# Kernel tuning notes

Measured on AMD Instinct MI355X. Metric: run time of the kernel, lower is better.

Reference implementation:

```python
import math
import jax, jax.numpy as jnp
import numpy as np

B, T, C = 2, 384, 768
NH, RANK = 384, 1          # code requires rank==1 and num_heads==T (block_size)
HD = C // NH               # head dim = 2
SCALE = (1.0 / math.sqrt(HD)) * (RANK ** 0.5)
LN_EPS = 1e-5


def _layernorm(x, g, b):
    m = jnp.mean(x, axis=-1, keepdims=True)
    v = jnp.mean(jnp.square(x - m), axis=-1, keepdims=True)
    return (x - m) * jax.lax.rsqrt(v + LN_EPS) * g + b


def setup_inputs() -> dict:
    key = jax.random.key(0)
    ks = jax.random.split(key, 8)
    s = 0.02
    return {
        "x": jax.random.normal(ks[0], (B, T, C), jnp.float32),
        "W_qkv": jax.random.normal(ks[1], (C, 3 * C), jnp.float32) * s,
        "b_qkv": jnp.zeros((3 * C,), jnp.float32),
        "W_proj": jax.random.normal(ks[2], (C, C), jnp.float32) * s,
        "b_proj": jnp.zeros((C,), jnp.float32),
        "ln1_g": jnp.ones((C,), jnp.float32),
        "ln1_b": jnp.zeros((C,), jnp.float32),
        "ln2_g": jnp.ones((C,), jnp.float32),
        "ln2_b": jnp.zeros((C,), jnp.float32),
        "W1": jax.random.normal(ks[3], (C, 4 * C), jnp.float32) * s,
        "b1": jnp.zeros((4 * C,), jnp.float32),
        "W2": jax.random.normal(ks[4], (4 * C, C), jnp.float32) * s,
        "b2": jnp.zeros((C,), jnp.float32),
    }


def reference(x, W_qkv, b_qkv, W_proj, b_proj, ln1_g, ln1_b, ln2_g, ln2_b, W1, b1, W2, b2):
    # --- attention branch (pre-LN) ---
    h = _layernorm(x, ln1_g, ln1_b)
    qkv = h @ W_qkv + b_qkv                       # [B,T,3C]
    q, k, v = jnp.split(qkv, 3, axis=-1)

    def split_heads(t):                           # [B,T,C] -> [B,RANK,T,NH,HD]
        return t.reshape(B, T, RANK, NH, HD).transpose(0, 2, 1, 3, 4)

    q, k, v = split_heads(q), split_heads(k), split_heads(v)
    # scores over the HEAD axis (nh x nh), per (batch, rank, time) -- faithful to source
    att = jnp.einsum('brtnd,brtmd->brtnm', q, k) * SCALE   # [B,RANK,T,NH,NH]
    tril = jnp.tril(jnp.ones((T, T), bool))       # NH == T so this broadcasts on (nh, nh)
    att = jnp.where(tril, att, -jnp.inf)
    att = jax.nn.softmax(att, axis=-1)
    y = jnp.einsum('brtnm,brtmd->brtnd', att, v)  # [B,RANK,T,NH,HD]
    y = y.transpose(0, 2, 1, 3, 4).reshape(B, T, C)
    x = x + (y @ W_proj + b_proj)

    # --- feed-forward branch: Linear -> Linear -> GELU (order faithful to source) ---
    h2 = _layernorm(x, ln2_g, ln2_b)
    ff = jax.nn.gelu((h2 @ W1 + b1) @ W2 + b2, approximate=False)
    return x + ff
```

## Files before the change

kernel.cpp:

```cpp
#include <hip/hip_runtime.h>
#include <hip/hip_bf16.h>
#include <math.h>

#define SCALE_QK 0.70710678118654752f
#define PSTRIDE 589824

typedef __attribute__((ext_vector_type(8))) short bf16x8;
typedef __attribute__((ext_vector_type(4))) float floatx4;

__device__ __forceinline__ void gload16(const void* g, void* l) {
  __builtin_amdgcn_global_load_lds(
      (const __attribute__((address_space(1))) void*)g,
      (__attribute__((address_space(3))) void*)l, 16, 0, 0);
}

__device__ __forceinline__ float bf2f(unsigned short u) {
  union { float f; unsigned int i; } c; c.i = ((unsigned int)u) << 16; return c.f;
}

__device__ __forceinline__ float gelu_f(float v) {
  return 0.5f * v * (1.f + erff(v * 0.70710678118654752f));
}

struct MegaArgs {
  const float *x, *Wq, *bq, *Wp, *bp, *g1, *be1, *g2, *be2, *W1, *b1, *W2, *b2;
  __hip_bfloat16 *h1, *qkvb, *yb, *h2, *ff1b, *Tq, *Tp, *T1, *T2;
  float *x2, *part, *out;
};

__device__ __forceinline__ void wconv_seg(const float* __restrict__ src,
                                          __hip_bfloat16* __restrict__ dst,
                                          int K, int N, int idx, char* smem) {
  float (*t)[33] = (float(*)[33])smem;
  int tilesN = N >> 5;
  int tk = idx / tilesN, tn = idx - tk * tilesN;
  int r = threadIdx.x >> 5, c = threadIdx.x & 31;
#pragma unroll
  for (int p = 0; p < 4; ++p)
    t[p * 8 + r][c] = src[(size_t)(tk * 32 + p * 8 + r) * N + tn * 32 + c];
  __syncthreads();
#pragma unroll
  for (int p = 0; p < 4; ++p)
    dst[(size_t)(tn * 32 + p * 8 + r) * K + tk * 32 + c] =
        __float2bfloat16(t[c][p * 8 + r]);
}

__device__ __forceinline__ void ln_row(const float* __restrict__ src,
                                       const float* __restrict__ g,
                                       const float* __restrict__ b,
                                       __hip_bfloat16* __restrict__ dst,
                                       int r, char* smem) {
  float* red0 = (float*)smem; float* red1 = red0 + 4;
  const float* xr = src + (size_t)r * 768;
  __hip_bfloat16* orow = dst + (size_t)r * 768;
  float vals[3]; float s = 0.f, s2 = 0.f;
#pragma unroll
  for (int p = 0; p < 3; ++p) {
    float v = xr[threadIdx.x + p * 256];
    vals[p] = v; s += v; s2 += v * v;
  }
#pragma unroll
  for (int off = 32; off > 0; off >>= 1) {
    s += __shfl_down(s, off); s2 += __shfl_down(s2, off);
  }
  int wid = threadIdx.x >> 6, lane = threadIdx.x & 63;
  if (lane == 0) { red0[wid] = s; red1[wid] = s2; }
  __syncthreads();
  if (threadIdx.x == 0) {
    red0[0] = red0[0] + red0[1] + red0[2] + red0[3];
    red1[0] = red1[0] + red1[1] + red1[2] + red1[3];
  }
  __syncthreads();
  float mean = red0[0] * (1.f / 768), var = red1[0] * (1.f / 768) - mean * mean;
  float rstd = rsqrtf(var + 1e-5f);
#pragma unroll
  for (int p = 0; p < 3; ++p) {
    int i = threadIdx.x + p * 256;
    orow[i] = __float2bfloat16((vals[p] - mean) * rstd * g[i] + b[i]);
  }
}

template <int NT, bool GELU, bool RES, bool OUT_BF16, bool SPLIT>
__device__ __forceinline__ void gemm_tile(
    const __hip_bfloat16* __restrict__ A, int ldA,
    const __hip_bfloat16* __restrict__ Bt, int ldB,
    const float* __restrict__ bias, const float* __restrict__ res,
    void* __restrict__ outp, int N, int bm, int bn, int kofe, char* lds) {
  const int tid = threadIdx.x;
  const int w = tid >> 6, l = tid & 63;

  const int sr = (w << 3) + (l >> 3);
  const int swb = ((l & 7) << 4) ^ ((l >> 3) << 4);
  const char* a0 = (const char*)(A + (size_t)(bm + sr) * ldA + kofe) + swb;
  const char* a1 = a0 + (size_t)32 * ldA * 2;
  const char* b0 = (const char*)(Bt + (size_t)(bn + sr) * ldB + kofe) + swb;
  const char* b1 = b0 + (size_t)32 * ldB * 2;
  char* dW = lds + (w << 10);

#define STAGE(buf, t) do {                     \
    char* d_ = dW + (buf) * 16384;             \
    gload16(a0 + (t) * 128, d_);               \
    gload16(a1 + (t) * 128, d_ + 4096);        \
    gload16(b0 + (t) * 128, d_ + 8192);        \
    gload16(b1 + (t) * 128, d_ + 12288);       \
  } while (0)

  const int wr = w >> 1, wc = w & 1;
  const int fr = l & 15, g = l >> 4;
  const int fsw = (fr & 7) << 4;
  int aof[2][2], bof[2][2];
#pragma unroll
  for (int i = 0; i < 2; ++i)
#pragma unroll
    for (int kk = 0; kk < 2; ++kk) {
      aof[i][kk] = (wr * 32 + i * 16 + fr) * 128 + ((kk * 64 + g * 16) ^ fsw);
      bof[i][kk] = 8192 + (wc * 32 + i * 16 + fr) * 128 +
                   ((kk * 64 + g * 16) ^ fsw);
    }

  floatx4 acc[2][2] = {};

#define COMPUTE(bufoff) do {                                          \
    const char* base_ = lds + (bufoff);                               \
    bf16x8 av_[2][2], bv_[2][2];                                      \
    _Pragma("unroll") for (int i = 0; i < 2; ++i)                     \
      _Pragma("unroll") for (int kk = 0; kk < 2; ++kk) {              \
        av_[i][kk] = *(const bf16x8*)(base_ + aof[i][kk]);            \
        bv_[i][kk] = *(const bf16x8*)(base_ + bof[i][kk]);            \
      }                                                               \
    _Pragma("unroll") for (int kk = 0; kk < 2; ++kk)                  \
      _Pragma("unroll") for (int i = 0; i < 2; ++i)                   \
        _Pragma("unroll") for (int j = 0; j < 2; ++j)                 \
          acc[i][j] = __builtin_amdgcn_mfma_f32_16x16x32_bf16(        \
              av_[i][kk], bv_[j][kk], acc[i][j], 0, 0, 0);            \
  } while (0)

  STAGE(0, 0);
  STAGE(1, 1);
  asm volatile("s_waitcnt vmcnt(4)" ::: "memory");
  __builtin_amdgcn_s_barrier();
  asm volatile("" ::: "memory");

#pragma unroll
  for (int t = 0; t < NT; ++t) {
    if (t + 2 < NT) STAGE((t + 2) % 3, t + 2);
    COMPUTE((t % 3) * 16384);
    if (t + 1 < NT) {
      if (t + 2 < NT) {
        asm volatile("s_waitcnt vmcnt(4)" ::: "memory");
      } else {
        asm volatile("s_waitcnt vmcnt(0)" ::: "memory");
      }
      __builtin_amdgcn_s_barrier();
      asm volatile("" ::: "memory");
    }
  }
#undef STAGE
#undef COMPUTE

  const int orow0 = bm + wr * 32 + g * 4;
  const int ocol0 = bn + wc * 32 + fr;
#pragma unroll
  for (int fm = 0; fm < 2; ++fm)
#pragma unroll
    for (int fn = 0; fn < 2; ++fn) {
      int col = ocol0 + fn * 16;
      float bv = SPLIT ? 0.f : bias[col];
#pragma unroll
      for (int i = 0; i < 4; ++i) {
        int row = orow0 + fm * 16 + i;
        if (SPLIT) {
          ((float*)outp)[(size_t)row * N + col] = acc[fm][fn][i];
        } else {
          float v = acc[fm][fn][i] + bv;
          if (GELU) v = gelu_f(v);
          if (RES) v += res[(size_t)row * N + col];
          if (OUT_BF16)
            ((__hip_bfloat16*)outp)[(size_t)row * N + col] = __float2bfloat16(v);
          else
            ((float*)outp)[(size_t)row * N + col] = v;
        }
      }
    }
}

__device__ __forceinline__ void attn_row(int n, const ushort2* base,
    const float2* ks, const float2* vs, __hip_bfloat16* yrow) {
  ushort2 qu = base[n];
  float q0 = bf2f(qu.x) * SCALE_QK, q1 = bf2f(qu.y) * SCALE_QK;
  float sm = 0.f, y0 = 0.f, y1 = 0.f;
  for (int m = 0; m <= n; ++m) {
    float2 km = ks[m], vm = vs[m];
    float p = __expf(fmaf(q0, km.x, q1 * km.y));
    sm += p;
    y0 = fmaf(p, vm.x, y0);
    y1 = fmaf(p, vm.y, y1);
  }
  float inv = 1.f / sm;
  yrow[2 * n]     = __float2bfloat16(y0 * inv);
  yrow[2 * n + 1] = __float2bfloat16(y1 * inv);
}

__device__ __forceinline__ void attn_token(int r, const MegaArgs& a, char* smem) {
  float2* ks = (float2*)smem;
  float2* vs = ks + 384;
  const int t = threadIdx.x;
  const ushort2* base = (const ushort2*)(a.qkvb + (size_t)r * 2304);
  {
    ushort2 ku = base[384 + t], vu = base[768 + t];
    ks[t] = make_float2(bf2f(ku.x), bf2f(ku.y));
    vs[t] = make_float2(bf2f(vu.x), bf2f(vu.y));
    if (t < 128) {
      ushort2 ku2 = base[384 + 256 + t], vu2 = base[768 + 256 + t];
      ks[256 + t] = make_float2(bf2f(ku2.x), bf2f(ku2.y));
      vs[256 + t] = make_float2(bf2f(vu2.x), bf2f(vu2.y));
    }
  }
  __syncthreads();
  __hip_bfloat16* yrow = a.yb + (size_t)r * 768;
  attn_row(t, base, ks, vs, yrow);
  if (t < 128) attn_row(383 - t, base, ks, vs, yrow);
}

__device__ __forceinline__ void p7_elem(int idx, const MegaArgs& a) {
  int i = idx * 4;
  floatx4 s = *(const floatx4*)(a.part + i);
  s += *(const floatx4*)(a.part + PSTRIDE + i);
  s += *(const floatx4*)(a.part + 2 * (size_t)PSTRIDE + i);
  s += *(const floatx4*)(a.part + 3 * (size_t)PSTRIDE + i);
  int c = i - (i / 768) * 768;
  floatx4 bv = *(const floatx4*)(a.b2 + c);
  floatx4 xv = *(const floatx4*)(a.x2 + i);
  floatx4 o;
#pragma unroll
  for (int e = 0; e < 4; ++e) o[e] = xv[e] + gelu_f(s[e] + bv[e]);
  *(floatx4*)(a.out + i) = o;
}

__global__ __launch_bounds__(256) void p0_k(MegaArgs a) {
  __shared__ __align__(16) char smem[8448];
  int j = blockIdx.x;
  if (j < 1728) wconv_seg(a.Wq, a.Tq, 768, 2304, j, smem);
  else          ln_row(a.x, a.g1, a.be1, a.h1, j - 1728, smem);
}
__global__ __launch_bounds__(256) void p1_k(MegaArgs a) {
  __shared__ __align__(16) char smem[49152];
  int j = blockIdx.x;
  if (j < 432) {
    int bm = (j / 36) << 6, bn = (j % 36) << 6;
    gemm_tile<12, false, false, true, false>(
        a.h1, 768, a.Tq, 768, a.bq, nullptr, a.qkvb, 2304, bm, bn, 0, smem);
  } else {
    int jj = j - 432;
    if (jj < 576)       wconv_seg(a.Wp, a.Tp, 768, 768, jj, smem);
    else if (jj < 2880) wconv_seg(a.W1, a.T1, 768, 3072, jj - 576, smem);
    else                wconv_seg(a.W2, a.T2, 3072, 768, jj - 2880, smem);
  }
}
__global__ __launch_bounds__(256) void p2_k(MegaArgs a) {
  __shared__ __align__(16) char smem[6144];
  attn_token(blockIdx.x, a, smem);
}
__global__ __launch_bounds__(256) void p3_k(MegaArgs a) {
  __shared__ __align__(16) char smem[49152];
  int j = blockIdx.x;
  int bm = (j / 12) << 6, bn = (j % 12) << 6;
  gemm_tile<12, false, true, false, false>(
      a.yb, 768, a.Tp, 768, a.bp, a.x, a.x2, 768, bm, bn, 0, smem);
}
__global__ __launch_bounds__(256) void p4_k(MegaArgs a) {
  __shared__ __align__(16) char smem[64];
  ln_row(a.x2, a.g2, a.be2, a.h2, blockIdx.x, smem);
}
__global__ __launch_bounds__(256) void p5_k(MegaArgs a) {
  __shared__ __align__(16) char smem[49152];
  int j = blockIdx.x;
  int bm = (j / 48) << 6, bn = (j % 48) << 6;
  gemm_tile<12, false, false, true, false>(
      a.h2, 768, a.T1, 768, a.b1, nullptr, a.ff1b, 3072, bm, bn, 0, smem);
}
__global__ __launch_bounds__(256) void p6_k(MegaArgs a) {
  __shared__ __align__(16) char smem[49152];
  int j = blockIdx.x;
  int z = j / 144, r2 = j - z * 144;
  int bm = (r2 / 12) << 6, bn = (r2 % 12) << 6;
  gemm_tile<12, false, false, false, true>(
      a.ff1b, 3072, a.T2, 3072, nullptr, nullptr,
      a.part + (size_t)z * PSTRIDE, 768, bm, bn, z * 768, smem);
}
__global__ __launch_bounds__(256) void p7_k(MegaArgs a) {
  p7_elem(blockIdx.x * 256 + threadIdx.x, a);
}

extern "C" void kernel_launch(void* const* d_in, const int* in_sizes, int n_in,
                              void* d_out, int out_size, void* d_ws,
                              size_t ws_size, hipStream_t stream) {
  (void)in_sizes; (void)n_in; (void)out_size; (void)ws_size;
  MegaArgs a;
  a.x   = (const float*)d_in[0];
  a.Wq  = (const float*)d_in[1];
  a.bq  = (const float*)d_in[2];
  a.Wp  = (const float*)d_in[3];
  a.bp  = (const float*)d_in[4];
  a.g1  = (const float*)d_in[5];
  a.be1 = (const float*)d_in[6];
  a.g2  = (const float*)d_in[7];
  a.be2 = (const float*)d_in[8];
  a.W1  = (const float*)d_in[9];
  a.b1  = (const float*)d_in[10];
  a.W2  = (const float*)d_in[11];
  a.b2  = (const float*)d_in[12];

  char* p = (char*)d_ws;
  a.h1   = (__hip_bfloat16*)p; p += 768 * 768 * 2;
  a.qkvb = (__hip_bfloat16*)p; p += 768 * 2304 * 2;
  a.yb   = (__hip_bfloat16*)p; p += 768 * 768 * 2;
  a.x2   = (float*)p;          p += 768 * 768 * 4;
  a.h2   = (__hip_bfloat16*)p; p += 768 * 768 * 2;
  a.ff1b = (__hip_bfloat16*)p; p += 768 * 3072 * 2;
  a.Tq   = (__hip_bfloat16*)p; p += 2304 * 768 * 2;
  a.Tp   = (__hip_bfloat16*)p; p += 768 * 768 * 2;
  a.T1   = (__hip_bfloat16*)p; p += 3072 * 768 * 2;
  a.T2   = (__hip_bfloat16*)p; p += 768 * 3072 * 2;
  a.part = (float*)p;          p += 4 * 768 * 768 * 4;
  a.out  = (float*)d_out;

  p0_k<<<2496, 256, 0, stream>>>(a);
  p1_k<<<5616, 256, 0, stream>>>(a);
  p2_k<<<768, 256, 0, stream>>>(a);
  p3_k<<<144, 256, 0, stream>>>(a);
  p4_k<<<768, 256, 0, stream>>>(a);
  p5_k<<<576, 256, 0, stream>>>(a);
  p6_k<<<576, 256, 0, stream>>>(a);
  p7_k<<<576, 256, 0, stream>>>(a);
}
```

Before: 85.90 us.

## Fuse LN2 and final GELU epilogue into GEMMs via last-block atomic counters

Removes the standalone LN2 and split-K reduction/GELU kernels. Each proj-GEMM row panel counts finished tiles with an atomic counter, and the last tile block runs layernorm for that 64-row panel. Likewise, the last of the four split-K partial blocks for each output tile reduces the partials and applies bias, GELU and the residual. This cuts two kernel launches and their gaps, at the cost of serialized tail work in the winning blocks and a counter reset added to the first kernel.

```diff
diff --git a/kernel.cpp b/kernel.cpp
--- a/kernel.cpp
+++ b/kernel.cpp
@@ -26,6 +26,7 @@
   const float *x, *Wq, *bq, *Wp, *bp, *g1, *be1, *g2, *be2, *W1, *b1, *W2, *b2;
   __hip_bfloat16 *h1, *qkvb, *yb, *h2, *ff1b, *Tq, *Tp, *T1, *T2;
   float *x2, *part, *out;
+  int *cnt;
 };
 
 __device__ __forceinline__ void wconv_seg(const float* __restrict__ src,
@@ -77,6 +78,53 @@
   for (int p = 0; p < 3; ++p) {
     int i = threadIdx.x + p * 256;
     orow[i] = __float2bfloat16((vals[p] - mean) * rstd * g[i] + b[i]);
+  }
+}
+
+__device__ __forceinline__ void ln_panel(const MegaArgs& a, int bm) {
+  const int sub = threadIdx.x & 3;
+  const int row = bm + (threadIdx.x >> 2);
+  const float* xr = a.x2 + (size_t)row * 768 + sub * 192;
+  float s = 0.f, s2 = 0.f;
+#pragma unroll
+  for (int i = 0; i < 48; ++i) {
+    floatx4 v = *(const floatx4*)(xr + i * 4);
+#pragma unroll
+    for (int e = 0; e < 4; ++e) { s += v[e]; s2 += v[e] * v[e]; }
+  }
+  s += __shfl_xor(s, 1); s2 += __shfl_xor(s2, 1);
+  s += __shfl_xor(s, 2); s2 += __shfl_xor(s2, 2);
+  float mean = s * (1.f / 768), var = s2 * (1.f / 768) - mean * mean;
+  float rstd = rsqrtf(var + 1e-5f);
+  __hip_bfloat16* orow = a.h2 + (size_t)row * 768 + sub * 192;
+  const float* g = a.g2 + sub * 192;
+  const float* b = a.be2 + sub * 192;
+#pragma unroll
+  for (int i = 0; i < 48; ++i) {
+    floatx4 v = *(const floatx4*)(xr + i * 4);
+#pragma unroll
+    for (int e = 0; e < 4; ++e)
+      orow[i * 4 + e] =
+          __float2bfloat16((v[e] - mean) * rstd * g[i * 4 + e] + b[i * 4 + e]);
+  }
+}
+
+__device__ __forceinline__ void ff2_finish(const MegaArgs& a, int bm, int bn) {
+#pragma unroll
+  for (int q = 0; q < 4; ++q) {
+    int e4 = q * 256 + threadIdx.x;
+    int r = e4 >> 4, c4 = e4 & 15;
+    size_t off = (size_t)(bm + r) * 768 + bn + c4 * 4;
+    floatx4 s = *(const floatx4*)(a.part + off);
+    s += *(const floatx4*)(a.part + PSTRIDE + off);
+    s += *(const floatx4*)(a.part + 2 * (size_t)PSTRIDE + off);
+    s += *(const floatx4*)(a.part + 3 * (size_t)PSTRIDE + off);
+    floatx4 bv = *(const floatx4*)(a.b2 + bn + c4 * 4);
+    floatx4 xv = *(const floatx4*)(a.x2 + off);
+    floatx4 o;
+#pragma unroll
+    for (int e = 0; e < 4; ++e) o[e] = xv[e] + gelu_f(s[e] + bv[e]);
+    *(floatx4*)(a.out + off) = o;
   }
 }
 
@@ -222,26 +270,12 @@
   if (t < 128) attn_row(383 - t, base, ks, vs, yrow);
 }
 
-__device__ __forceinline__ void p7_elem(int idx, const MegaArgs& a) {
-  int i = idx * 4;
-  floatx4 s = *(const floatx4*)(a.part + i);
-  s += *(const floatx4*)(a.part + PSTRIDE + i);
-  s += *(const floatx4*)(a.part + 2 * (size_t)PSTRIDE + i);
-  s += *(const floatx4*)(a.part + 3 * (size_t)PSTRIDE + i);
-  int c = i - (i / 768) * 768;
-  floatx4 bv = *(const floatx4*)(a.b2 + c);
-  floatx4 xv = *(const floatx4*)(a.x2 + i);
-  floatx4 o;
-#pragma unroll
-  for (int e = 0; e < 4; ++e) o[e] = xv[e] + gelu_f(s[e] + bv[e]);
-  *(floatx4*)(a.out + i) = o;
-}
-
 __global__ __launch_bounds__(256) void p0_k(MegaArgs a) {
   __shared__ __align__(16) char smem[8448];
   int j = blockIdx.x;
-  if (j < 1728) wconv_seg(a.Wq, a.Tq, 768, 2304, j, smem);
-  else          ln_row(a.x, a.g1, a.be1, a.h1, j - 1728, smem);
+  if (j < 1728)      wconv_seg(a.Wq, a.Tq, 768, 2304, j, smem);
+  else if (j < 2496) ln_row(a.x, a.g1, a.be1, a.h1, j - 1728, smem);
+  else if (threadIdx.x < 156) a.cnt[threadIdx.x] = 0;
 }
 __global__ __launch_bounds__(256) void p1_k(MegaArgs a) {
   __shared__ __align__(16) char smem[49152];
@@ -263,33 +297,44 @@
 }
 __global__ __launch_bounds__(256) void p3_k(MegaArgs a) {
   __shared__ __align__(16) char smem[49152];
+  __shared__ int winner;
   int j = blockIdx.x;
   int bm = (j / 12) << 6, bn = (j % 12) << 6;
   gemm_tile<12, false, true, false, false>(
       a.yb, 768, a.Tp, 768, a.bp, a.x, a.x2, 768, bm, bn, 0, smem);
+  __syncthreads();
+  __threadfence();
+  if (threadIdx.x == 0) winner = atomicAdd(&a.cnt[bm >> 6], 1);
+  __syncthreads();
+  if (winner == 11) {
+    __threadfence();
+    ln_panel(a, bm);
+  }
 }
 __global__ __launch_bounds__(256) void p4_k(MegaArgs a) {
-  __shared__ __align__(16) char smem[64];
-  ln_row(a.x2, a.g2, a.be2, a.h2, blockIdx.x, smem);
-}
-__global__ __launch_bounds__(256) void p5_k(MegaArgs a) {
   __shared__ __align__(16) char smem[49152];
   int j = blockIdx.x;
   int bm = (j / 48) << 6, bn = (j % 48) << 6;
   gemm_tile<12, false, false, true, false>(
       a.h2, 768, a.T1, 768, a.b1, nullptr, a.ff1b, 3072, bm, bn, 0, smem);
 }
-__global__ __launch_bounds__(256) void p6_k(MegaArgs a) {
+__global__ __launch_bounds__(256) void p5_k(MegaArgs a) {
   __shared__ __align__(16) char smem[49152];
+  __shared__ int winner;
   int j = blockIdx.x;
   int z = j / 144, r2 = j - z * 144;
   int bm = (r2 / 12) << 6, bn = (r2 % 12) << 6;
   gemm_tile<12, false, false, false, true>(
       a.ff1b, 3072, a.T2, 3072, nullptr, nullptr,
       a.part + (size_t)z * PSTRIDE, 768, bm, bn, z * 768, smem);
-}
-__global__ __launch_bounds__(256) void p7_k(MegaArgs a) {
-  p7_elem(blockIdx.x * 256 + threadIdx.x, a);
+  __syncthreads();
+  __threadfence();
+  if (threadIdx.x == 0) winner = atomicAdd(&a.cnt[12 + r2], 1);
+  __syncthreads();
+  if (winner == 3) {
+    __threadfence();
+    ff2_finish(a, bm, bn);
+  }
 }
 
 extern "C" void kernel_launch(void* const* d_in, const int* in_sizes, int n_in,
@@ -323,14 +368,13 @@
   a.T1   = (__hip_bfloat16*)p; p += 3072 * 768 * 2;
   a.T2   = (__hip_bfloat16*)p; p += 768 * 3072 * 2;
   a.part = (float*)p;          p += 4 * 768 * 768 * 4;
+  a.cnt  = (int*)p;            p += 156 * 4;
   a.out  = (float*)d_out;
 
-  p0_k<<<2496, 256, 0, stream>>>(a);
+  p0_k<<<2497, 256, 0, stream>>>(a);
   p1_k<<<5616, 256, 0, stream>>>(a);
   p2_k<<<768, 256, 0, stream>>>(a);
   p3_k<<<144, 256, 0, stream>>>(a);
-  p4_k<<<768, 256, 0, stream>>>(a);
+  p4_k<<<576, 256, 0, stream>>>(a);
   p5_k<<<576, 256, 0, stream>>>(a);
-  p6_k<<<576, 256, 0, stream>>>(a);
-  p7_k<<<576, 256, 0, stream>>>(a);
-}
+}
```

Result: slower. 231.9 us (+170.0%).
